# Optimization experiments

Hardware: AMD Instinct MI355X
Metric: run time of the kernel (lower is better)

## Reference

```python
import jax, jax.numpy as jnp
import numpy as np

TEMPERATURE = 32.0  # sqrt(d_model=1024)

def setup_inputs() -> dict:
    key = jax.random.key(0)
    kq, kk, kv = jax.random.split(key, 3)
    B, H, S, D = 2, 16, 2048, 64
    q = jax.random.normal(kq, (B, H, S, D), dtype=jnp.float32)
    k = jax.random.normal(kk, (B, H, S, D), dtype=jnp.float32)
    v = jax.random.normal(kv, (B, H, S, D), dtype=jnp.float32)
    mask = jnp.ones((B, 1, 1, S), dtype=jnp.int32)  # key-padding mask, 1 = keep
    return {"q": q, "k": k, "v": v, "mask": mask}

def reference(q, k, v, mask):
    # scores: [B,H,S,S]
    scores = jnp.einsum('bhqd,bhkd->bhqk', q / TEMPERATURE, k)
    scores = jnp.where(mask == 0, jnp.float32(-1e9), scores)
    attention = jax.nn.softmax(scores, axis=-1)
    # dropout is identity at inference (module's nn.Dropout in eval mode)
    output = jnp.einsum('bhqk,bhkd->bhqd', attention, v)
    return (output, attention)
```

## Files before the change

kernel.cpp:

```cpp
#include <hip/hip_runtime.h>
#include <hip/hip_bf16.h>


#define S_LEN 2048
#define D_DIM 64
#define BM 64
#define BN 64
#define NT (S_LEN / BN)
#define LDP 72
#define PSTR 136
#define BH_N 32
#define TILE_USH 4096

typedef __attribute__((ext_vector_type(8))) short bf16x8;
typedef __attribute__((ext_vector_type(4))) float f32x4;

__device__ __forceinline__ unsigned pack_bf16(float a, float b) {
    union { __hip_bfloat162 h; unsigned u; } cv;
    cv.h = __float22bfloat162_rn(make_float2(a, b));
    return cv.u;
}
__device__ __forceinline__ unsigned short bf1(float x) {
    union { __hip_bfloat16 h; unsigned short u; } cv;
    cv.h = __float2bfloat16(x);
    return cv.u;
}
__device__ __forceinline__ float bf2f(unsigned bits) {
    return __uint_as_float(bits);
}

__global__ __launch_bounds__(256)
void conv_k(const float* __restrict__ Kg, unsigned short* __restrict__ Kw) {
    const int kt = blockIdx.x;
    const int bh = blockIdx.y;
    const int tid = threadIdx.x;
    const float* Kb = Kg + ((size_t)bh * S_LEN + kt * 64) * D_DIM;
    unsigned short* Ko = Kw + ((size_t)bh * NT + kt) * TILE_USH;
    #pragma unroll
    for (int i = 0; i < 2; ++i) {
        int c = tid + i * 256;
        int l15 = c & 15, quad = (c >> 4) & 3, ks = (c >> 6) & 1, cb = (c >> 7) & 3;
        const float* src = Kb + (cb * 16 + l15) * D_DIM + ks * 32 + quad * 8;
        const float4 a = *(const float4*)src;
        const float4 b = *(const float4*)(src + 4);
        uint4 o;
        o.x = pack_bf16(a.x, a.y);
        o.y = pack_bf16(a.z, a.w);
        o.z = pack_bf16(b.x, b.y);
        o.w = pack_bf16(b.z, b.w);
        *(uint4*)(Ko + (size_t)c * 8) = o;
    }
}

__global__ __launch_bounds__(256)
void conv_vt(const float* __restrict__ Vg, unsigned short* __restrict__ Vtw) {
    const int bh = blockIdx.y;
    const int d  = threadIdx.x & 63;
    const int kq = threadIdx.x >> 6;
    const int key0 = blockIdx.x * 32 + kq * 8;
    const float* Vb = Vg + ((size_t)bh * S_LEN + key0) * D_DIM + d;
    float f[8];
    #pragma unroll
    for (int i = 0; i < 8; ++i) f[i] = Vb[i * D_DIM];
    uint4 o;
    o.x = pack_bf16(f[0], f[1]);
    o.y = pack_bf16(f[2], f[3]);
    o.z = pack_bf16(f[4], f[5]);
    o.w = pack_bf16(f[6], f[7]);
    const int kt  = key0 >> 6;
    const int ko  = key0 & 63;
    const int ks2 = ko >> 5, quad = (ko >> 3) & 3;
    const int db  = d >> 4,  l15  = d & 15;
    const int c   = db * 128 + ks2 * 64 + quad * 16 + l15;
    *(uint4*)(Vtw + ((size_t)bh * NT + kt) * TILE_USH + (size_t)c * 8) = o;
}

template <int PRE>
__global__ __launch_bounds__(256, 4)
void attn_kernel(const float* __restrict__ Qg, const float* __restrict__ Kg,
                 const float* __restrict__ Vg, const int* __restrict__ Mg,
                 const unsigned short* __restrict__ Kw,
                 const unsigned short* __restrict__ Vtw,
                 float* __restrict__ Og, float* __restrict__ Ag) {
    __shared__ unsigned short Ks[BN * LDP];
    __shared__ unsigned short QV[D_DIM * LDP];
    __shared__ unsigned short Pb[BM * PSTR];
    __shared__ int maskS[BN];

    const int tid  = threadIdx.x;
    const int w    = tid >> 6;
    const int lane = tid & 63;
    const int l15  = lane & 15;
    const int quad = lane >> 4;

    const int qt = blockIdx.x;
    const int bh = blockIdx.y;
    const int b  = bh >> 4;
    const int q0 = qt * BM;
    const int qrow = w * 16 + l15;

    const float* Qb = Qg + ((size_t)bh * S_LEN + q0) * D_DIM;
    const int*   Mb = Mg + (size_t)b * S_LEN;
    float* Ob = Og + ((size_t)bh * S_LEN + q0) * D_DIM;
    float* Ab = Ag + ((size_t)bh * S_LEN + q0) * (size_t)S_LEN;

    {
        const float sc = 0.04508422f;
        #pragma unroll
        for (int i = 0; i < 4; ++i) {
            int f = tid + i * 256;
            int row = f >> 4, c4 = f & 15;
            const float4 v = *(const float4*)(Qb + row * D_DIM + c4 * 4);
            *(uint2*)(&QV[row * LDP + c4 * 4]) =
                make_uint2(pack_bf16(v.x * sc, v.y * sc), pack_bf16(v.z * sc, v.w * sc));
        }
    }
    __syncthreads();

    bf16x8 aq[2];
    #pragma unroll
    for (int ks = 0; ks < 2; ++ks)
        aq[ks] = *(const bf16x8*)(&QV[qrow * LDP + ks * 32 + quad * 8]);

    auto stage_k = [&](int key0) {
        if constexpr (PRE) {
            const unsigned short* Kt = Kw + ((size_t)bh * NT + (key0 >> 6)) * TILE_USH;
            #pragma unroll
            for (int i = 0; i < 2; ++i) {
                int c = tid + i * 256;
                uint4 vv = *(const uint4*)(Kt + (size_t)c * 8);
                int l15c = c & 15, quadc = (c >> 4) & 3, ksc = (c >> 6) & 1, cbc = (c >> 7) & 3;
                *(uint4*)(&Ks[(cbc * 16 + l15c) * LDP + ksc * 32 + quadc * 8]) = vv;
            }
        } else {
            const float* Kb = Kg + ((size_t)bh * S_LEN + key0) * D_DIM;
            #pragma unroll
            for (int i = 0; i < 4; ++i) {
                int f = tid + i * 256;
                int row = f >> 4, c4 = f & 15;
                const float4 v = *(const float4*)(Kb + row * D_DIM + c4 * 4);
                *(uint2*)(&Ks[row * LDP + c4 * 4]) =
                    make_uint2(pack_bf16(v.x, v.y), pack_bf16(v.z, v.w));
            }
        }
    };
    auto stage_v = [&](int key0) {
        if constexpr (PRE) {
            const unsigned short* Vt = Vtw + ((size_t)bh * NT + (key0 >> 6)) * TILE_USH;
            #pragma unroll
            for (int i = 0; i < 2; ++i) {
                int c = tid + i * 256;
                uint4 vv = *(const uint4*)(Vt + (size_t)c * 8);
                int l15c = c & 15, quadc = (c >> 4) & 3, ks2c = (c >> 6) & 1, dbc = (c >> 7) & 3;
                *(uint4*)(&QV[(dbc * 16 + l15c) * LDP + ks2c * 32 + quadc * 8]) = vv;
            }
        } else {
            int key = tid & 63, g2 = tid >> 6;
            #pragma unroll
            for (int i = 0; i < 4; ++i) {
                int d0 = (g2 * 4 + i) * 4;
                const float4 v = *(const float4*)(Vg + ((size_t)bh * S_LEN + key0 + key) * D_DIM + d0);
                QV[(d0 + 0) * LDP + key] = bf1(v.x);
                QV[(d0 + 1) * LDP + key] = bf1(v.y);
                QV[(d0 + 2) * LDP + key] = bf1(v.z);
                QV[(d0 + 3) * LDP + key] = bf1(v.w);
            }
        }
    };

    float lsum = 0.f;

    if constexpr (PRE) {
        const unsigned short* Kb = Kw + (size_t)bh * NT * TILE_USH;
        for (int kt = 0; kt < NT; ++kt) {
            const unsigned short* Kt = Kb + (size_t)kt * TILE_USH + lane * 8;
            const int* Mt = Mb + kt * BN + quad * 4;
            #pragma unroll
            for (int cb = 0; cb < 4; ++cb) {
                f32x4 acc = {0.f, 0.f, 0.f, 0.f};
                #pragma unroll
                for (int ks = 0; ks < 2; ++ks) {
                    bf16x8 bk = *(const bf16x8*)(Kt + cb * 1024 + ks * 512);
                    acc = __builtin_amdgcn_mfma_f32_16x16x32_bf16(bk, aq[ks], acc, 0, 0, 0);
                }
                const int4 m4 = *(const int4*)(Mt + cb * 16);
                float e0 = m4.x ? __builtin_exp2f(acc[0]) : 0.f;
                float e1 = m4.y ? __builtin_exp2f(acc[1]) : 0.f;
                float e2 = m4.z ? __builtin_exp2f(acc[2]) : 0.f;
                float e3 = m4.w ? __builtin_exp2f(acc[3]) : 0.f;
                lsum += (e0 + e1) + (e2 + e3);
            }
        }
    } else {
        for (int kt = 0; kt < NT; ++kt) {
            const int key0 = kt * BN;
            stage_k(key0);
            if (tid < BN) maskS[tid] = Mb[key0 + tid];
            __syncthreads();
            #pragma unroll
            for (int cb = 0; cb < 4; ++cb) {
                f32x4 acc = {0.f, 0.f, 0.f, 0.f};
                #pragma unroll
                for (int ks = 0; ks < 2; ++ks) {
                    bf16x8 bk = *(const bf16x8*)(&Ks[(cb * 16 + l15) * LDP + ks * 32 + quad * 8]);
                    acc = __builtin_amdgcn_mfma_f32_16x16x32_bf16(bk, aq[ks], acc, 0, 0, 0);
                }
                const int4 m4 = *(const int4*)(&maskS[cb * 16 + quad * 4]);
                float e0 = m4.x ? __builtin_exp2f(acc[0]) : 0.f;
                float e1 = m4.y ? __builtin_exp2f(acc[1]) : 0.f;
                float e2 = m4.z ? __builtin_exp2f(acc[2]) : 0.f;
                float e3 = m4.w ? __builtin_exp2f(acc[3]) : 0.f;
                lsum += (e0 + e1) + (e2 + e3);
            }
            __syncthreads();
        }
    }

    lsum += __shfl_xor(lsum, 16);
    lsum += __shfl_xor(lsum, 32);
    const float linv = 1.0f / lsum;

    __syncthreads();

    f32x4 oacc[4];
    #pragma unroll
    for (int db = 0; db < 4; ++db) oacc[db] = (f32x4){0.f, 0.f, 0.f, 0.f};

    for (int kt2 = 0; kt2 < NT / 2; ++kt2) {
        #pragma unroll
        for (int half = 0; half < 2; ++half) {
            const int key0 = (kt2 * 2 + half) * BN;
            stage_k(key0);
            stage_v(key0);
            if (tid < BN) maskS[tid] = Mb[key0 + tid];
            __syncthreads();

            #pragma unroll
            for (int cb = 0; cb < 4; ++cb) {
                f32x4 acc = {0.f, 0.f, 0.f, 0.f};
                #pragma unroll
                for (int ks = 0; ks < 2; ++ks) {
                    bf16x8 bk = *(const bf16x8*)(&Ks[(cb * 16 + l15) * LDP + ks * 32 + quad * 8]);
                    acc = __builtin_amdgcn_mfma_f32_16x16x32_bf16(bk, aq[ks], acc, 0, 0, 0);
                }
                const int4 m4 = *(const int4*)(&maskS[cb * 16 + quad * 4]);
                float p0 = (m4.x ? __builtin_exp2f(acc[0]) : 0.f) * linv;
                float p1 = (m4.y ? __builtin_exp2f(acc[1]) : 0.f) * linv;
                float p2 = (m4.z ? __builtin_exp2f(acc[2]) : 0.f) * linv;
                float p3 = (m4.w ? __builtin_exp2f(acc[3]) : 0.f) * linv;
                *(uint2*)(&Pb[qrow * PSTR + half * 64 + cb * 16 + quad * 4]) =
                    make_uint2(pack_bf16(p0, p1), pack_bf16(p2, p3));
            }

            #pragma unroll
            for (int ks2 = 0; ks2 < 2; ++ks2) {
                bf16x8 ap = *(const bf16x8*)(&Pb[qrow * PSTR + half * 64 + ks2 * 32 + quad * 8]);
                #pragma unroll
                for (int db = 0; db < 4; ++db) {
                    bf16x8 bv = *(const bf16x8*)(&QV[(db * 16 + l15) * LDP + ks2 * 32 + quad * 8]);
                    oacc[db] = __builtin_amdgcn_mfma_f32_16x16x32_bf16(bv, ap, oacc[db], 0, 0, 0);
                }
            }
            __syncthreads();
        }

        const int key00 = kt2 * 2 * BN;
        #pragma unroll
        for (int i = 0; i < 8; ++i) {
            int idx = tid + i * 256;
            int row = idx >> 5, c4 = idx & 31;
            uint2 pu = *(const uint2*)(&Pb[row * PSTR + c4 * 4]);
            f32x4 t;
            t[0] = bf2f(pu.x << 16); t[1] = bf2f(pu.x & 0xffff0000u);
            t[2] = bf2f(pu.y << 16); t[3] = bf2f(pu.y & 0xffff0000u);
            __builtin_nontemporal_store(
                t, (f32x4*)(Ab + (size_t)row * S_LEN + key00 + c4 * 4));
        }
    }

    #pragma unroll
    for (int db = 0; db < 4; ++db) {
        f32x4 o4 = oacc[db];
        __builtin_nontemporal_store(
            o4, (f32x4*)(Ob + (size_t)qrow * D_DIM + db * 16 + quad * 4));
    }
}

extern "C" void kernel_launch(void* const* d_in, const int* in_sizes, int n_in,
                              void* d_out, int out_size, void* d_ws, size_t ws_size,
                              hipStream_t stream) {
    const float* q = (const float*)d_in[0];
    const float* k = (const float*)d_in[1];
    const float* v = (const float*)d_in[2];
    const int* mask = (const int*)d_in[3];
    float* out = (float*)d_out;
    float* attn = out + (size_t)2 * 16 * 2048 * 64;

    const size_t kw_elems = (size_t)BH_N * S_LEN * D_DIM;
    const size_t need = 2 * kw_elems * sizeof(unsigned short);
    dim3 block(256);
    dim3 grid(S_LEN / BM, BH_N);

    if (d_ws && ws_size >= need) {
        unsigned short* Kw  = (unsigned short*)d_ws;
        unsigned short* Vtw = Kw + kw_elems;
        conv_k<<<dim3(NT, BH_N), block, 0, stream>>>(k, Kw);
        conv_vt<<<dim3(S_LEN / 32, BH_N), block, 0, stream>>>(v, Vtw);
        attn_kernel<1><<<grid, block, 0, stream>>>(q, k, v, mask, Kw, Vtw, out, attn);
    } else {
        attn_kernel<0><<<grid, block, 0, stream>>>(q, k, v, mask, nullptr, nullptr, out, attn);
    }
}
```

Before: 628.1 us.

## Read pre-swizzled K/V fragments directly from global in attention pass two

Splits the templated kernel into a fast kernel and a fallback. In the fast kernel, the second pass loads K and V MFMA fragments directly from the pre-laid-out global buffers instead of staging them through shared memory. This removes the per-tile shared-memory copies and block-wide barriers and shrinks the LDS footprint. The trade-off is redundant global/L2 traffic, since each wave now fetches the full K/V tiles itself.

```diff
diff --git a/kernel.cpp b/kernel.cpp
--- a/kernel.cpp
+++ b/kernel.cpp
@@ -75,17 +75,13 @@
     *(uint4*)(Vtw + ((size_t)bh * NT + kt) * TILE_USH + (size_t)c * 8) = o;
 }
 
-template <int PRE>
 __global__ __launch_bounds__(256, 4)
-void attn_kernel(const float* __restrict__ Qg, const float* __restrict__ Kg,
-                 const float* __restrict__ Vg, const int* __restrict__ Mg,
-                 const unsigned short* __restrict__ Kw,
-                 const unsigned short* __restrict__ Vtw,
-                 float* __restrict__ Og, float* __restrict__ Ag) {
-    __shared__ unsigned short Ks[BN * LDP];
-    __shared__ unsigned short QV[D_DIM * LDP];
+void attn_fast(const float* __restrict__ Qg, const int* __restrict__ Mg,
+               const unsigned short* __restrict__ Kw,
+               const unsigned short* __restrict__ Vtw,
+               float* __restrict__ Og, float* __restrict__ Ag) {
+    __shared__ unsigned short Qs[BM * LDP];
     __shared__ unsigned short Pb[BM * PSTR];
-    __shared__ int maskS[BN];
 
     const int tid  = threadIdx.x;
     const int w    = tid >> 6;
@@ -104,6 +100,9 @@
     float* Ob = Og + ((size_t)bh * S_LEN + q0) * D_DIM;
     float* Ab = Ag + ((size_t)bh * S_LEN + q0) * (size_t)S_LEN;
 
+    const unsigned short* KbF = Kw  + (size_t)bh * NT * TILE_USH;
+    const unsigned short* VbF = Vtw + (size_t)bh * NT * TILE_USH;
+
     {
         const float sc = 0.04508422f;
         #pragma unroll
@@ -111,7 +110,7 @@
             int f = tid + i * 256;
             int row = f >> 4, c4 = f & 15;
             const float4 v = *(const float4*)(Qb + row * D_DIM + c4 * 4);
-            *(uint2*)(&QV[row * LDP + c4 * 4]) =
+            *(uint2*)(&Qs[row * LDP + c4 * 4]) =
                 make_uint2(pack_bf16(v.x * sc, v.y * sc), pack_bf16(v.z * sc, v.w * sc));
         }
     }
@@ -120,61 +119,44 @@
     bf16x8 aq[2];
     #pragma unroll
     for (int ks = 0; ks < 2; ++ks)
-        aq[ks] = *(const bf16x8*)(&QV[qrow * LDP + ks * 32 + quad * 8]);
-
-    auto stage_k = [&](int key0) {
-        if constexpr (PRE) {
-            const unsigned short* Kt = Kw + ((size_t)bh * NT + (key0 >> 6)) * TILE_USH;
-            #pragma unroll
-            for (int i = 0; i < 2; ++i) {
-                int c = tid + i * 256;
-                uint4 vv = *(const uint4*)(Kt + (size_t)c * 8);
-                int l15c = c & 15, quadc = (c >> 4) & 3, ksc = (c >> 6) & 1, cbc = (c >> 7) & 3;
-                *(uint4*)(&Ks[(cbc * 16 + l15c) * LDP + ksc * 32 + quadc * 8]) = vv;
-            }
-        } else {
-            const float* Kb = Kg + ((size_t)bh * S_LEN + key0) * D_DIM;
-            #pragma unroll
-            for (int i = 0; i < 4; ++i) {
-                int f = tid + i * 256;
-                int row = f >> 4, c4 = f & 15;
-                const float4 v = *(const float4*)(Kb + row * D_DIM + c4 * 4);
-                *(uint2*)(&Ks[row * LDP + c4 * 4]) =
-                    make_uint2(pack_bf16(v.x, v.y), pack_bf16(v.z, v.w));
-            }
-        }
-    };
-    auto stage_v = [&](int key0) {
-        if constexpr (PRE) {
-            const unsigned short* Vt = Vtw + ((size_t)bh * NT + (key0 >> 6)) * TILE_USH;
-            #pragma unroll
-            for (int i = 0; i < 2; ++i) {
-                int c = tid + i * 256;
-                uint4 vv = *(const uint4*)(Vt + (size_t)c * 8);
-                int l15c = c & 15, quadc = (c >> 4) & 3, ks2c = (c >> 6) & 1, dbc = (c >> 7) & 3;
-                *(uint4*)(&QV[(dbc * 16 + l15c) * LDP + ks2c * 32 + quadc * 8]) = vv;
-            }
-        } else {
-            int key = tid & 63, g2 = tid >> 6;
-            #pragma unroll
-            for (int i = 0; i < 4; ++i) {
-                int d0 = (g2 * 4 + i) * 4;
-                const float4 v = *(const float4*)(Vg + ((size_t)bh * S_LEN + key0 + key) * D_DIM + d0);
-                QV[(d0 + 0) * LDP + key] = bf1(v.x);
-                QV[(d0 + 1) * LDP + key] = bf1(v.y);
-                QV[(d0 + 2) * LDP + key] = bf1(v.z);
-                QV[(d0 + 3) * LDP + key] = bf1(v.w);
-            }
-        }
-    };
+        aq[ks] = *(const bf16x8*)(&Qs[qrow * LDP + ks * 32 + quad * 8]);
 
     float lsum = 0.f;
-
-    if constexpr (PRE) {
-        const unsigned short* Kb = Kw + (size_t)bh * NT * TILE_USH;
-        for (int kt = 0; kt < NT; ++kt) {
-            const unsigned short* Kt = Kb + (size_t)kt * TILE_USH + lane * 8;
+    for (int kt = 0; kt < NT; ++kt) {
+        const unsigned short* Kt = KbF + (size_t)kt * TILE_USH + lane * 8;
+        const int* Mt = Mb + kt * BN + quad * 4;
+        #pragma unroll
+        for (int cb = 0; cb < 4; ++cb) {
+            f32x4 acc = {0.f, 0.f, 0.f, 0.f};
+            #pragma unroll
+            for (int ks = 0; ks < 2; ++ks) {
+                bf16x8 bk = *(const bf16x8*)(Kt + cb * 1024 + ks * 512);
+                acc = __builtin_amdgcn_mfma_f32_16x16x32_bf16(bk, aq[ks], acc, 0, 0, 0);
+            }
+            const int4 m4 = *(const int4*)(Mt + cb * 16);
+            float e0 = m4.x ? __builtin_exp2f(acc[0]) : 0.f;
+            float e1 = m4.y ? __builtin_exp2f(acc[1]) : 0.f;
+            float e2 = m4.z ? __builtin_exp2f(acc[2]) : 0.f;
+            float e3 = m4.w ? __builtin_exp2f(acc[3]) : 0.f;
+            lsum += (e0 + e1) + (e2 + e3);
+        }
+    }
+    lsum += __shfl_xor(lsum, 16);
+    lsum += __shfl_xor(lsum, 32);
+    const float linv = 1.0f / lsum;
+
+    f32x4 oacc[4];
+    #pragma unroll
+    for (int db = 0; db < 4; ++db) oacc[db] = (f32x4){0.f, 0.f, 0.f, 0.f};
+
+    for (int kt2 = 0; kt2 < NT / 2; ++kt2) {
+        #pragma unroll
+        for (int half = 0; half < 2; ++half) {
+            const int kt = kt2 * 2 + half;
+            const unsigned short* Kt = KbF + (size_t)kt * TILE_USH + lane * 8;
+            const unsigned short* Vt = VbF + (size_t)kt * TILE_USH + lane * 8;
             const int* Mt = Mb + kt * BN + quad * 4;
+
             #pragma unroll
             for (int cb = 0; cb < 4; ++cb) {
                 f32x4 acc = {0.f, 0.f, 0.f, 0.f};
@@ -184,43 +166,141 @@
                     acc = __builtin_amdgcn_mfma_f32_16x16x32_bf16(bk, aq[ks], acc, 0, 0, 0);
                 }
                 const int4 m4 = *(const int4*)(Mt + cb * 16);
-                float e0 = m4.x ? __builtin_exp2f(acc[0]) : 0.f;
-                float e1 = m4.y ? __builtin_exp2f(acc[1]) : 0.f;
-                float e2 = m4.z ? __builtin_exp2f(acc[2]) : 0.f;
-                float e3 = m4.w ? __builtin_exp2f(acc[3]) : 0.f;
-                lsum += (e0 + e1) + (e2 + e3);
-            }
-        }
-    } else {
-        for (int kt = 0; kt < NT; ++kt) {
-            const int key0 = kt * BN;
-            stage_k(key0);
-            if (tid < BN) maskS[tid] = Mb[key0 + tid];
-            __syncthreads();
-            #pragma unroll
-            for (int cb = 0; cb < 4; ++cb) {
-                f32x4 acc = {0.f, 0.f, 0.f, 0.f};
+                float p0 = (m4.x ? __builtin_exp2f(acc[0]) : 0.f) * linv;
+                float p1 = (m4.y ? __builtin_exp2f(acc[1]) : 0.f) * linv;
+                float p2 = (m4.z ? __builtin_exp2f(acc[2]) : 0.f) * linv;
+                float p3 = (m4.w ? __builtin_exp2f(acc[3]) : 0.f) * linv;
+                *(uint2*)(&Pb[qrow * PSTR + half * 64 + cb * 16 + quad * 4]) =
+                    make_uint2(pack_bf16(p0, p1), pack_bf16(p2, p3));
+            }
+
+            #pragma unroll
+            for (int ks2 = 0; ks2 < 2; ++ks2) {
+                bf16x8 ap = *(const bf16x8*)(&Pb[qrow * PSTR + half * 64 + ks2 * 32 + quad * 8]);
                 #pragma unroll
-                for (int ks = 0; ks < 2; ++ks) {
-                    bf16x8 bk = *(const bf16x8*)(&Ks[(cb * 16 + l15) * LDP + ks * 32 + quad * 8]);
-                    acc = __builtin_amdgcn_mfma_f32_16x16x32_bf16(bk, aq[ks], acc, 0, 0, 0);
+                for (int db = 0; db < 4; ++db) {
+                    bf16x8 bv = *(const bf16x8*)(Vt + db * 1024 + ks2 * 512);
+                    oacc[db] = __builtin_amdgcn_mfma_f32_16x16x32_bf16(bv, ap, oacc[db], 0, 0, 0);
                 }
-                const int4 m4 = *(const int4*)(&maskS[cb * 16 + quad * 4]);
-                float e0 = m4.x ? __builtin_exp2f(acc[0]) : 0.f;
-                float e1 = m4.y ? __builtin_exp2f(acc[1]) : 0.f;
-                float e2 = m4.z ? __builtin_exp2f(acc[2]) : 0.f;
-                float e3 = m4.w ? __builtin_exp2f(acc[3]) : 0.f;
-                lsum += (e0 + e1) + (e2 + e3);
-            }
-            __syncthreads();
-        }
-    }
-
+            }
+        }
+
+        const int key00 = kt2 * 2 * BN;
+        #pragma unroll
+        for (int i = 0; i < 8; ++i) {
+            const int row = w * 16 + i * 2 + (lane >> 5);
+            const int c4  = lane & 31;
+            uint2 pu = *(const uint2*)(&Pb[row * PSTR + c4 * 4]);
+            f32x4 t;
+            t[0] = bf2f(pu.x << 16); t[1] = bf2f(pu.x & 0xffff0000u);
+            t[2] = bf2f(pu.y << 16); t[3] = bf2f(pu.y & 0xffff0000u);
+            __builtin_nontemporal_store(
+                t, (f32x4*)(Ab + (size_t)row * S_LEN + key00 + c4 * 4));
+        }
+    }
+
+    #pragma unroll
+    for (int db = 0; db < 4; ++db) {
+        f32x4 o4 = oacc[db];
+        __builtin_nontemporal_store(
+            o4, (f32x4*)(Ob + (size_t)qrow * D_DIM + db * 16 + quad * 4));
+    }
+}
+
+__global__ __launch_bounds__(256, 4)
+void attn_fallback(const float* __restrict__ Qg, const float* __restrict__ Kg,
+                   const float* __restrict__ Vg, const int* __restrict__ Mg,
+                   float* __restrict__ Og, float* __restrict__ Ag) {
+    __shared__ unsigned short Ks[BN * LDP];
+    __shared__ unsigned short QV[D_DIM * LDP];
+    __shared__ unsigned short Pb[BM * PSTR];
+    __shared__ int maskS[BN];
+
+    const int tid  = threadIdx.x;
+    const int w    = tid >> 6;
+    const int lane = tid & 63;
+    const int l15  = lane & 15;
+    const int quad = lane >> 4;
+
+    const int qt = blockIdx.x;
+    const int bh = blockIdx.y;
+    const int b  = bh >> 4;
+    const int q0 = qt * BM;
+    const int qrow = w * 16 + l15;
+
+    const float* Qb = Qg + ((size_t)bh * S_LEN + q0) * D_DIM;
+    const int*   Mb = Mg + (size_t)b * S_LEN;
+    float* Ob = Og + ((size_t)bh * S_LEN + q0) * D_DIM;
+    float* Ab = Ag + ((size_t)bh * S_LEN + q0) * (size_t)S_LEN;
+
+    {
+        const float sc = 0.04508422f;
+        #pragma unroll
+        for (int i = 0; i < 4; ++i) {
+            int f = tid + i * 256;
+            int row = f >> 4, c4 = f & 15;
+            const float4 v = *(const float4*)(Qb + row * D_DIM + c4 * 4);
+            *(uint2*)(&QV[row * LDP + c4 * 4]) =
+                make_uint2(pack_bf16(v.x * sc, v.y * sc), pack_bf16(v.z * sc, v.w * sc));
+        }
+    }
+    __syncthreads();
+
+    bf16x8 aq[2];
+    #pragma unroll
+    for (int ks = 0; ks < 2; ++ks)
+        aq[ks] = *(const bf16x8*)(&QV[qrow * LDP + ks * 32 + quad * 8]);
+
+    auto stage_k = [&](int key0) {
+        const float* Kb = Kg + ((size_t)bh * S_LEN + key0) * D_DIM;
+        #pragma unroll
+        for (int i = 0; i < 4; ++i) {
+            int f = tid + i * 256;
+            int row = f >> 4, c4 = f & 15;
+            const float4 v = *(const float4*)(Kb + row * D_DIM + c4 * 4);
+            *(uint2*)(&Ks[row * LDP + c4 * 4]) =
+                make_uint2(pack_bf16(v.x, v.y), pack_bf16(v.z, v.w));
+        }
+    };
+    auto stage_v = [&](int key0) {
+        int key = tid & 63, g2 = tid >> 6;
+        #pragma unroll
+        for (int i = 0; i < 4; ++i) {
+            int d0 = (g2 * 4 + i) * 4;
+            const float4 v = *(const float4*)(Vg + ((size_t)bh * S_LEN + key0 + key) * D_DIM + d0);
+            QV[(d0 + 0) * LDP + key] = bf1(v.x);
+            QV[(d0 + 1) * LDP + key] = bf1(v.y);
+            QV[(d0 + 2) * LDP + key] = bf1(v.z);
+            QV[(d0 + 3) * LDP + key] = bf1(v.w);
+        }
+    };
+
+    float lsum = 0.f;
+    for (int kt = 0; kt < NT; ++kt) {
+        const int key0 = kt * BN;
+        stage_k(key0);
+        if (tid < BN) maskS[tid] = Mb[key0 + tid];
+        __syncthreads();
+        #pragma unroll
+        for (int cb = 0; cb < 4; ++cb) {
+            f32x4 acc = {0.f, 0.f, 0.f, 0.f};
+            #pragma unroll
+            for (int ks = 0; ks < 2; ++ks) {
+                bf16x8 bk = *(const bf16x8*)(&Ks[(cb * 16 + l15) * LDP + ks * 32 + quad * 8]);
+                acc = __builtin_amdgcn_mfma_f32_16x16x32_bf16(bk, aq[ks], acc, 0, 0, 0);
+            }
+            const int4 m4 = *(const int4*)(&maskS[cb * 16 + quad * 4]);
+            float e0 = m4.x ? __builtin_exp2f(acc[0]) : 0.f;
+            float e1 = m4.y ? __builtin_exp2f(acc[1]) : 0.f;
+            float e2 = m4.z ? __builtin_exp2f(acc[2]) : 0.f;
+            float e3 = m4.w ? __builtin_exp2f(acc[3]) : 0.f;
+            lsum += (e0 + e1) + (e2 + e3);
+        }
+        __syncthreads();
+    }
     lsum += __shfl_xor(lsum, 16);
     lsum += __shfl_xor(lsum, 32);
     const float linv = 1.0f / lsum;
-
-    __syncthreads();
 
     f32x4 oacc[4];
     #pragma unroll
@@ -306,8 +386,8 @@
         unsigned short* Vtw = Kw + kw_elems;
         conv_k<<<dim3(NT, BH_N), block, 0, stream>>>(k, Kw);
         conv_vt<<<dim3(S_LEN / 32, BH_N), block, 0, stream>>>(v, Vtw);
-        attn_kernel<1><<<grid, block, 0, stream>>>(q, k, v, mask, Kw, Vtw, out, attn);
+        attn_fast<<<grid, block, 0, stream>>>(q, mask, Kw, Vtw, out, attn);
     } else {
-        attn_kernel<0><<<grid, block, 0, stream>>>(q, k, v, mask, nullptr, nullptr, out, attn);
-    }
-}
+        attn_fallback<<<grid, block, 0, stream>>>(q, k, v, mask, out, attn);
+    }
+}
```

Result: slower. 644.5 us (+2.6%).
